# Performance work log

Measured on AMD Instinct MI355X. Metric: run time of the kernel, lower is better.

The kernel has to match this reference:

```python
import jax, jax.numpy as jnp
import numpy as np

NUM_HEADS = 16
WINDOW = 128


def apply_rope(x):
    # x: (B, H, S, Dh), standard RoPE with half-split rotation, base 10000
    S, Dh = x.shape[-2], x.shape[-1]
    half = Dh // 2
    inv_freq = 1.0 / (10000.0 ** (jnp.arange(half, dtype=jnp.float32) / half))
    ang = jnp.arange(S, dtype=jnp.float32)[:, None] * inv_freq[None, :]  # (S, half)
    cos, sin = jnp.cos(ang), jnp.sin(ang)
    x1, x2 = x[..., :half], x[..., half:]
    return jnp.concatenate([x1 * cos - x2 * sin, x1 * sin + x2 * cos], axis=-1).astype(x.dtype)


def setup_inputs() -> dict:
    key = jax.random.key(0)
    ks = jax.random.split(key, 5)
    D = 1024
    B, S = 2, 2048
    w = 0.02
    return {
        "x": jax.random.normal(ks[0], (B, S, D), dtype=jnp.float32),
        "Wq": jax.random.normal(ks[1], (D, D), dtype=jnp.float32) * w,
        "bq": jnp.zeros((D,), dtype=jnp.float32),
        "Wk": jax.random.normal(ks[2], (D, D), dtype=jnp.float32) * w,
        "bk": jnp.zeros((D,), dtype=jnp.float32),
        "Wv": jax.random.normal(ks[3], (D, D), dtype=jnp.float32) * w,
        "bv": jnp.zeros((D,), dtype=jnp.float32),
        "Wo": jax.random.normal(ks[4], (D, D), dtype=jnp.float32) * w,
        "bo": jnp.zeros((D,), dtype=jnp.float32),
    }


def reference(x, Wq, bq, Wk, bk, Wv, bv, Wo, bo):
    B, S, D = x.shape
    H = NUM_HEADS
    Dh = D // H

    def proj(W, b):
        y = jnp.einsum("bsd,ed->bse", x, W) + b  # nn.Linear: x @ W.T + b
        return y.reshape(B, S, H, Dh).transpose(0, 2, 1, 3)  # (B,H,S,Dh)

    q = apply_rope(proj(Wq, bq)) * (Dh ** -0.5)
    k = apply_rope(proj(Wk, bk))
    v = proj(Wv, bv)

    scores = jnp.einsum("bhqd,bhkd->bhqk", q, k)  # (B,H,S,S)
    idx = jnp.arange(S)
    rel = idx[None, :] - idx[:, None]  # k - q
    blocked = (rel > 0) | (rel < -WINDOW)  # True = masked out
    scores = jnp.where(blocked[None, None], -jnp.inf, scores)
    probs = jax.nn.softmax(scores, axis=-1)
    out = jnp.einsum("bhqk,bhkd->bhqd", probs, v)
    out = out.transpose(0, 2, 1, 3).reshape(B, S, D)
    return jnp.einsum("bsd,ed->bse", out, Wo) + bo
```

## Files before the change

### kernel.cpp

```cpp
#include <hip/hip_runtime.h>

typedef __attribute__((ext_vector_type(8)))  __bf16 bf16x8;
typedef __attribute__((ext_vector_type(4)))  float  f32x4;

__device__ __forceinline__ short f2bf(float f) {
    unsigned u = __builtin_bit_cast(unsigned, f);
    unsigned r = (u + 0x7fffu + ((u >> 16) & 1u)) >> 16;
    return (short)r;
}
__device__ __forceinline__ float lo16(unsigned u) { return __builtin_bit_cast(float, u << 16); }
__device__ __forceinline__ float hi16(unsigned u) { return __builtin_bit_cast(float, u & 0xffff0000u); }

__device__ __forceinline__ void gload16(const void* g, void* l) {
    __builtin_amdgcn_global_load_lds(
        (const __attribute__((address_space(1))) unsigned*)g,
        (__attribute__((address_space(3))) unsigned*)l, 16, 0, 0);
}

__device__ __forceinline__ void ropePair(const uint4& a, const uint4& b,
                                         const float2* cs8, float scale,
                                         uint4& oa, uint4& ob) {
    const unsigned au[4] = {a.x, a.y, a.z, a.w}, bu[4] = {b.x, b.y, b.z, b.w};
    unsigned ra[4], rb[4];
    #pragma unroll
    for (int wi = 0; wi < 4; ++wi) {
        const float x1l = lo16(au[wi]), x1h = hi16(au[wi]);
        const float x2l = lo16(bu[wi]), x2h = hi16(bu[wi]);
        const float2 cl = cs8[wi * 2], ch = cs8[wi * 2 + 1];
        const float o1l = (x1l * cl.x - x2l * cl.y) * scale;
        const float o2l = (x1l * cl.y + x2l * cl.x) * scale;
        const float o1h = (x1h * ch.x - x2h * ch.y) * scale;
        const float o2h = (x1h * ch.y + x2h * ch.x) * scale;
        ra[wi] = (unsigned)(unsigned short)f2bf(o1l) | ((unsigned)(unsigned short)f2bf(o1h) << 16);
        rb[wi] = (unsigned)(unsigned short)f2bf(o2l) | ((unsigned)(unsigned short)f2bf(o2h) << 16);
    }
    oa = make_uint4(ra[0], ra[1], ra[2], ra[3]);
    ob = make_uint4(rb[0], rb[1], rb[2], rb[3]);
}

#define S_LEN   2048
#define MAT_ELEMS 4194304
#define VT_ROW  2176
#define VT_MAT  2228224

__global__ __launch_bounds__(256) void prep(
    const float* __restrict__ x,  const float* __restrict__ Wq,
    const float* __restrict__ Wk, const float* __restrict__ Wv,
    const float* __restrict__ Wo, const float* __restrict__ bq,
    const float* __restrict__ bk, const float* __restrict__ bv,
    short* __restrict__ xb, short* __restrict__ wcat, short* __restrict__ wob,
    float* __restrict__ bcat, float2* __restrict__ tab, short* __restrict__ vt)
{
    const int tid = blockIdx.x * 256 + threadIdx.x;
    const float4* src;
    short* dst;
    if (tid < 1048576) {
        src = (const float4*)x + tid;  dst = xb + (size_t)tid * 4;
    } else if (tid < 1835008) {
        const int o = tid - 1048576;
        const int mat = o >> 18;
        const int wi  = o & 262143;
        const float* W = (mat == 0) ? Wq : (mat == 1) ? Wk : Wv;
        src = (const float4*)W + wi;  dst = wcat + (size_t)o * 4;
    } else {
        const int o = tid - 1835008;
        src = (const float4*)Wo + o;  dst = wob + (size_t)o * 4;
    }
    const float4 v = *src;
    short4 s4 = make_short4(f2bf(v.x), f2bf(v.y), f2bf(v.z), f2bf(v.w));
    *(short4*)dst = s4;

    if (tid < 65536) {
        const int s  = tid >> 5;
        const int jr = tid & 31;
        const float freq = exp2f(-(float)jr * (13.287712379549449f / 32.0f));
        const float ang  = (float)s * freq;
        tab[tid] = make_float2(cosf(ang), sinf(ang));
    }
    if (tid < 768) {
        const float* B = (tid < 256) ? bq : (tid < 512) ? bk : bv;
        ((float4*)bcat)[tid] = ((const float4*)B)[tid & 255];
    }
    if (tid < 16384) {
        const int row = tid >> 3, ch = tid & 7;
        *(uint4*)&vt[(size_t)row * VT_ROW + ch * 8] = make_uint4(0, 0, 0, 0);
    }
}

#define VMC4 do { asm volatile("s_waitcnt vmcnt(4)" ::: "memory"); __builtin_amdgcn_sched_barrier(0); } while (0)
#define VMC0 do { asm volatile("s_waitcnt vmcnt(0)" ::: "memory"); __builtin_amdgcn_sched_barrier(0); } while (0)
#define BAR  __builtin_amdgcn_s_barrier()
#define SB   __builtin_amdgcn_sched_barrier(0)

#define LDA_ALL(T) _Pragma("unroll") for (int ii = 0; ii < 4; ++ii) { \
    aF[ii][0] = ldf(T, fA0, ii * 2048);                                \
    aF[ii][1] = ldf(T, fA1, ii * 2048); }
#define LDB0(T) _Pragma("unroll") for (int jj = 0; jj < 3; ++jj) {    \
    b0[jj][0] = ldf(T, fB0, jj * 2048);                                \
    b0[jj][1] = ldf(T, fB1, jj * 2048); }
#define LDB1(T) _Pragma("unroll") for (int jj = 0; jj < 3; ++jj) {    \
    b1[jj][0] = ldf(T, fB0, (jj + 3) * 2048);                          \
    b1[jj][1] = ldf(T, fB1, (jj + 3) * 2048); }

#define MFMA_HALF(JB, BQ)                                                     \
  __builtin_amdgcn_s_setprio(1);                                              \
  _Pragma("unroll") for (int ii = 0; ii < 4; ++ii)                            \
    _Pragma("unroll") for (int jj = 0; jj < 3; ++jj) {                        \
      acc[ii][(JB)+jj] = __builtin_amdgcn_mfma_f32_16x16x32_bf16(             \
          aF[ii][0], BQ[jj][0], acc[ii][(JB)+jj], 0, 0, 0);                   \
      acc[ii][(JB)+jj] = __builtin_amdgcn_mfma_f32_16x16x32_bf16(             \
          aF[ii][1], BQ[jj][1], acc[ii][(JB)+jj], 0, 0, 0);                   \
    }                                                                         \
  __builtin_amdgcn_s_setprio(0);

#define STGA(KT_, TILE) _Pragma("unroll") for (int g = 0; g < 4; ++g)  \
    gload16(gA + g * 16384 + (KT_) * 128, (TILE) + (w * 32 + g * 8) * 64);
#define STGB(KT_, TILE) _Pragma("unroll") for (int g = 0; g < 3; ++g)  \
    gload16(gB + g * 16384 + (KT_) * 128, (TILE) + (w * 24 + g * 8) * 64);

#define KT2(CA, CB, SBSTG, SASTG, WSTMT)              \
  LDA_ALL(CA); LDB0(CB); SBSTG;                       \
  MFMA_HALF(0, b0); SB; LDB1(CB); SB;                 \
  BAR;                                                \
  SASTG;                                              \
  MFMA_HALF(3, b1); WSTMT; BAR;

__global__ __launch_bounds__(512) void gemm8(
    const short* __restrict__ A,
    const short* __restrict__ Bw,
    const float* __restrict__ bias,
    short* __restrict__ outb,
    short* __restrict__ vt)
{
    __shared__ short lds[57344];
    short* const Ab0 = lds;
    short* const Bb0 = lds + 16384;
    short* const Ab1 = lds + 28672;
    short* const Bb1 = lds + 45056;

    const int tid = threadIdx.x;
    const int w = tid >> 6, lane = tid & 63;
    const int wm = w >> 1, wn = w & 1;
    const int lr = lane & 15, lg = lane >> 4;

    const int wg  = blockIdx.x;
    const int swz = (wg & 7) * 32 + (wg >> 3);
    const int bx = swz & 15, by = swz >> 4;
    const int row0 = by * 256, col0 = bx * 192;

    const int scl  = ((lane & 7) * 16) ^ (((lane >> 3) & 7) << 4);
    const int goff = (lane >> 3) * 2048 + scl;
    const char* gA = (const char*)A  + (size_t)(row0 + w * 32) * 2048 + goff;
    const char* gB = (const char*)Bw + (size_t)(col0 + w * 24) * 2048 + goff;
    const int cswz0 = (lg * 16)      ^ ((lr & 7) << 4);
    const int cswz1 = (64 + lg * 16) ^ ((lr & 7) << 4);
    const int fA0 = (wm * 64 + lr) * 128 + cswz0;
    const int fA1 = (wm * 64 + lr) * 128 + cswz1;
    const int fB0 = (wn * 96 + lr) * 128 + cswz0;
    const int fB1 = (wn * 96 + lr) * 128 + cswz1;

    auto ldf = [&](const short* buf, int voff, int imm) -> bf16x8 {
        return *(const bf16x8*)((const char*)buf + voff + imm);
    };

    f32x4 acc[4][6] = {};
    bf16x8 aF[4][2], b0[3][2], b1[3][2];

    STGA(0, Ab0); STGB(0, Bb0); STGA(1, Ab1);
    VMC4;
    BAR;

    #pragma unroll 1
    for (int it = 0; it < 7; ++it) {
        const int t0 = it * 2;
        KT2(Ab0, Bb0, STGB(t0 + 1, Bb1), STGA(t0 + 2, Ab0), VMC4)
        const int t1 = t0 + 1;
        KT2(Ab1, Bb1, STGB(t1 + 1, Bb0), STGA(t1 + 2, Ab1), VMC4)
    }
    KT2(Ab0, Bb0, STGB(15, Bb1), {}, VMC0)
    KT2(Ab1, Bb1, {}, {}, {})

    #pragma unroll
    for (int j = 0; j < 6; ++j) {
        const int base_cm = col0 + wn * 96 + j * 16;
        const int matj = base_cm >> 10;
        const float bb = bias[base_cm + lr];
        if (matj == 2) {
            const size_t dgo = (size_t)(base_cm - 2048 + lr) * VT_ROW;
            #pragma unroll
            for (int i = 0; i < 4; ++i) {
                const int rg = row0 + wm * 64 + i * 16 + lg * 4;
                const int bq_ = rg >> 11, key = rg & 2047;
                short4 sv;
                sv.x = f2bf(acc[i][j][0] + bb); sv.y = f2bf(acc[i][j][1] + bb);
                sv.z = f2bf(acc[i][j][2] + bb); sv.w = f2bf(acc[i][j][3] + bb);
                *(short4*)&vt[(size_t)bq_ * VT_MAT + dgo + 128 + key] = sv;
            }
        } else {
            short* outm = outb + (size_t)matj * MAT_ELEMS;
            const int cmod = (base_cm & 1023) + lr;
            #pragma unroll
            for (int i = 0; i < 4; ++i) {
                const int rg = row0 + wm * 64 + i * 16 + lg * 4;
                #pragma unroll
                for (int r = 0; r < 4; ++r)
                    outm[(size_t)(rg + r) * 1024 + cmod] = f2bf(acc[i][j][r] + bb);
            }
        }
    }
}

__global__ __launch_bounds__(256) void gemm_out(
    const short* __restrict__ A, const short* __restrict__ Bw,
    const float* __restrict__ bias, float* __restrict__ outf)
{
    __shared__ short As[128 * 64];
    __shared__ short Bs[64 * 64];
    const int tid  = threadIdx.x;
    const int w    = tid >> 6, lane = tid & 63;
    const int row0 = blockIdx.y * 128, col0 = blockIdx.x * 64;
    const int lr   = lane & 15, lg = lane >> 4;
    const int srow = lane >> 3, scol = (lane & 7) * 8;

    f32x4 acc[2][4] = {};

    for (int kt = 0; kt < 16; ++kt) {
        const int k0 = kt * 64;
        __syncthreads();
        #pragma unroll
        for (int rr = 0; rr < 4; ++rr) {
            const int r = w * 32 + rr * 8;
            gload16(A + (size_t)(row0 + r + srow) * 1024 + k0 + scol, (short*)As + r * 64);
        }
        #pragma unroll
        for (int rr = 0; rr < 2; ++rr) {
            const int r = w * 16 + rr * 8;
            gload16(Bw + (size_t)(col0 + r + srow) * 1024 + k0 + scol, (short*)Bs + r * 64);
        }
        __syncthreads();
        #pragma unroll
        for (int kk = 0; kk < 2; ++kk) {
            const int kb = kk * 32 + lg * 8;
            bf16x8 af[2], bf[4];
            #pragma unroll
            for (int i = 0; i < 2; ++i)
                af[i] = *(const bf16x8*)&As[(w * 32 + i * 16 + lr) * 64 + kb];
            #pragma unroll
            for (int j = 0; j < 4; ++j)
                bf[j] = *(const bf16x8*)&Bs[(j * 16 + lr) * 64 + kb];
            #pragma unroll
            for (int i = 0; i < 2; ++i)
                #pragma unroll
                for (int j = 0; j < 4; ++j)
                    acc[i][j] = __builtin_amdgcn_mfma_f32_16x16x32_bf16(af[i], bf[j], acc[i][j], 0, 0, 0);
        }
    }

    #pragma unroll
    for (int i = 0; i < 2; ++i) {
        const int grb = row0 + w * 32 + i * 16 + lg * 4;
        #pragma unroll
        for (int j = 0; j < 4; ++j) {
            const int cm = col0 + j * 16 + lr;
            const float bb = bias[cm];
            #pragma unroll
            for (int r = 0; r < 4; ++r)
                outf[(size_t)(grb + r) * 1024 + cm] = acc[i][j][r] + bb;
        }
    }
}

#define KS_ST 72
#define P_ST  168
__global__ __launch_bounds__(512) void attn_mfma(const short* __restrict__ qkv,
                                                 const short* __restrict__ vt,
                                                 short* __restrict__ ctx,
                                                 const float2* __restrict__ tab)
{
    __shared__ char lds[76800];
    short* Ks  = (short*)lds;
    short* Pl  = (short*)lds;
    char*  VTs = lds + 43008;
    float* linv = (float*)(lds + 75776);

    const int tid = threadIdx.x;
    const int w = tid >> 6, lane = tid & 63;
    const int g = lane >> 4, l15 = lane & 15;
    const int phys = blockIdx.x;
    const int bid = (phys & 7) * 64 + (phys >> 3);
    const int b  = bid >> 8;
    const int h  = (bid >> 4) & 15;
    const int qb = bid & 15;
    const int qs = qb << 7;
    const size_t rowbase = (size_t)b * S_LEN;
    const int hc = h << 6;

    const short* vhead = vt + ((size_t)b * 1024 + h * 64) * VT_ROW + qs;
    #pragma unroll
    for (int rdx = 0; rdx < 4; ++rdx) {
        const int c = rdx * 512 + tid;
        const int row = c >> 5, ch = c & 31;
        const int srcb = (ch * 16) ^ ((row & 7) << 4);
        gload16((const char*)(vhead + (size_t)row * VT_ROW) + srcb, VTs + c * 16);
    }

    #pragma unroll
    for (int it = 0; it < 2; ++it) {
        const int c   = it * 512 + tid;
        const int key = c >> 2;
        const int jb  = (c & 3) << 3;
        const int gk  = qs - 128 + key;
        const int gkc = gk < 0 ? 0 : gk;
        const short* kb = qkv + (size_t)1 * MAT_ELEMS + (rowbase + gkc) * 1024 + hc;
        const uint4 k1 = *(const uint4*)(kb + jb);
        const uint4 k2 = *(const uint4*)(kb + jb + 32);
        uint4 o1, o2;
        ropePair(k1, k2, tab + (size_t)gkc * 32 + jb, 1.0f, o1, o2);
        if (gk < 0) { o1 = make_uint4(0, 0, 0, 0); o2 = make_uint4(0, 0, 0, 0); }
        *(uint4*)&Ks[key * KS_ST + jb]      = o1;
        *(uint4*)&Ks[key * KS_ST + jb + 32] = o2;
    }
    __syncthreads();

    const int q = qs + 16 * w + l15;
    const size_t qoff = (rowbase + q) * 1024 + hc;
    const uint4 q1 = *(const uint4*)&qkv[qoff + g * 8];
    const uint4 q2 = *(const uint4*)&qkv[qoff + 32 + g * 8];
    uint4 r1, r2;
    ropePair(q1, q2, tab + (size_t)q * 32 + g * 8, 0.125f, r1, r2);
    const bf16x8 qf0 = __builtin_bit_cast(bf16x8, r1);
    const bf16x8 qf1 = __builtin_bit_cast(bf16x8, r2);

    f32x4 st[9];
    #pragma unroll
    for (int t = 0; t < 9; ++t) {
        const int krow = 16 * w + 16 * t + l15;
        bf16x8 kf0 = *(const bf16x8*)&Ks[krow * KS_ST + g * 8];
        bf16x8 kf1 = *(const bf16x8*)&Ks[krow * KS_ST + 32 + g * 8];
        f32x4 a = {0.f, 0.f, 0.f, 0.f};
        a = __builtin_amdgcn_mfma_f32_16x16x32_bf16(qf0, kf0, a, 0, 0, 0);
        a = __builtin_amdgcn_mfma_f32_16x16x32_bf16(qf1, kf1, a, 0, 0, 0);
        st[t] = a;
    }
    __syncthreads();

    const int jmin = 128 - qs - 16 * w;
    float mrow[4], lsum[4];
    #pragma unroll
    for (int r = 0; r < 4; ++r) mrow[r] = -3.0e38f;
    #pragma unroll
    for (int t = 0; t < 9; ++t) {
        const int jj = 16 * t + l15;
        #pragma unroll
        for (int r = 0; r < 4; ++r) {
            const int qi = 4 * g + r;
            const bool ok = (jj >= qi) && (jj <= qi + 128) && (jj >= jmin);
            if (ok) mrow[r] = fmaxf(mrow[r], st[t][r]);
        }
    }
    #pragma unroll
    for (int r = 0; r < 4; ++r) {
        mrow[r] = fmaxf(mrow[r], __shfl_xor(mrow[r], 1));
        mrow[r] = fmaxf(mrow[r], __shfl_xor(mrow[r], 2));
        mrow[r] = fmaxf(mrow[r], __shfl_xor(mrow[r], 4));
        mrow[r] = fmaxf(mrow[r], __shfl_xor(mrow[r], 8));
        lsum[r] = 0.0f;
    }
    short* Pw = Pl + w * (16 * P_ST);
    #pragma unroll
    for (int t = 0; t < 9; ++t) {
        const int jj = 16 * t + l15;
        #pragma unroll
        for (int r = 0; r < 4; ++r) {
            const int qi = 4 * g + r;
            const bool ok = (jj >= qi) && (jj <= qi + 128) && (jj >= jmin);
            const float p = ok ? __expf(st[t][r] - mrow[r]) : 0.0f;
            lsum[r] += p;
            Pw[qi * P_ST + jj] = f2bf(p);
        }
    }
    {
        short4 z = make_short4(0, 0, 0, 0);
        *(short4*)&Pw[l15 * P_ST + 144 + 4 * g] = z;
    }
    #pragma unroll
    for (int r = 0; r < 4; ++r) {
        lsum[r] += __shfl_xor(lsum[r], 1);
        lsum[r] += __shfl_xor(lsum[r], 2);
        lsum[r] += __shfl_xor(lsum[r], 4);
        lsum[r] += __shfl_xor(lsum[r], 8);
        if (l15 == r) linv[w * 16 + 4 * g + r] = 1.0f / lsum[r];
    }

    f32x4 oc[4] = {};
    #pragma unroll
    for (int kc = 0; kc < 5; ++kc) {
        bf16x8 pf = *(const bf16x8*)&Pw[l15 * P_ST + kc * 32 + g * 8];
        int cole = 16 * w + kc * 32 + g * 8;
        if (cole > 248) cole = 248;
        const int colb = cole * 2;
        #pragma unroll
        for (int dt = 0; dt < 4; ++dt) {
            const int row = dt * 16 + l15;
            bf16x8 vf = *(const bf16x8*)(VTs + row * 512 + (colb ^ ((row & 7) << 4)));
            oc[dt] = __builtin_amdgcn_mfma_f32_16x16x32_bf16(vf, pf, oc[dt], 0, 0, 0);
        }
    }

    const float inv = linv[w * 16 + l15];
    #pragma unroll
    for (int dt = 0; dt < 4; ++dt) {
        short4 sv;
        sv.x = f2bf(oc[dt][0] * inv);
        sv.y = f2bf(oc[dt][1] * inv);
        sv.z = f2bf(oc[dt][2] * inv);
        sv.w = f2bf(oc[dt][3] * inv);
        *(short4*)&ctx[(rowbase + qs + 16 * w + l15) * 1024 + hc + dt * 16 + 4 * g] = sv;
    }
}

extern "C" void kernel_launch(void* const* d_in, const int* in_sizes, int n_in,
                              void* d_out, int out_size, void* d_ws, size_t ws_size,
                              hipStream_t stream) {
    const float* x  = (const float*)d_in[0];
    const float* Wq = (const float*)d_in[1];
    const float* bq = (const float*)d_in[2];
    const float* Wk = (const float*)d_in[3];
    const float* bk = (const float*)d_in[4];
    const float* Wv = (const float*)d_in[5];
    const float* bv = (const float*)d_in[6];
    const float* Wo = (const float*)d_in[7];
    const float* bo = (const float*)d_in[8];

    char* ws = (char*)d_ws;
    short*  xb   = (short*) (ws + 0);
    short*  ctx  = (short*) (ws + 0);
    short*  wcat = (short*) (ws + 8388608);
    short*  wob  = (short*) (ws + 14680064);
    short*  qkv  = (short*) (ws + 16777216);
    short*  vt   = (short*) (ws + 33554432);
    float2* tab  = (float2*)(ws + 42467328);
    float*  bcat = (float*) (ws + 42991616);

    prep<<<8192, 256, 0, stream>>>(x, Wq, Wk, Wv, Wo, bq, bk, bv,
                                   xb, wcat, wob, bcat, tab, vt);
    gemm8<<<256, 512, 0, stream>>>(xb, wcat, bcat, qkv, vt);
    attn_mfma<<<512, 512, 0, stream>>>(qkv, vt, ctx, tab);
    gemm_out<<<dim3(16, 32), 256, 0, stream>>>(ctx, wob, bo, (float*)d_out);
}
```

Baseline: 80.74 us.

## Split GEMM k-step into four barrier-separated LDS-load/MFMA phases

Restructures the QKV projection GEMM main loop so each k-tile is processed in four quarters. Each quarter loads half of the A or B fragments from LDS and then runs a 2x3 MFMA block, with workgroup barriers between phases in a ping-pong style schedule. The aim is to interleave LDS reads with MFMA work across waves and reduce register pressure from holding all A fragments at once. The cost is many more s_barrier calls per k-step, and the explicit sched_barrier hints are removed.

```diff
diff --git a/kernel.cpp b/kernel.cpp
--- a/kernel.cpp
+++ b/kernel.cpp
@@ -90,26 +90,28 @@
 #define VMC4 do { asm volatile("s_waitcnt vmcnt(4)" ::: "memory"); __builtin_amdgcn_sched_barrier(0); } while (0)
 #define VMC0 do { asm volatile("s_waitcnt vmcnt(0)" ::: "memory"); __builtin_amdgcn_sched_barrier(0); } while (0)
 #define BAR  __builtin_amdgcn_s_barrier()
-#define SB   __builtin_amdgcn_sched_barrier(0)
-
-#define LDA_ALL(T) _Pragma("unroll") for (int ii = 0; ii < 4; ++ii) { \
-    aF[ii][0] = ldf(T, fA0, ii * 2048);                                \
+
+#define LDAL(T) _Pragma("unroll") for (int ii = 0; ii < 2; ++ii) { \
+    aF[ii][0] = ldf(T, fA0, ii * 2048);                             \
     aF[ii][1] = ldf(T, fA1, ii * 2048); }
-#define LDB0(T) _Pragma("unroll") for (int jj = 0; jj < 3; ++jj) {    \
-    b0[jj][0] = ldf(T, fB0, jj * 2048);                                \
+#define LDAH(T) _Pragma("unroll") for (int ii = 2; ii < 4; ++ii) { \
+    aF[ii][0] = ldf(T, fA0, ii * 2048);                             \
+    aF[ii][1] = ldf(T, fA1, ii * 2048); }
+#define LDBL(T) _Pragma("unroll") for (int jj = 0; jj < 3; ++jj) { \
+    b0[jj][0] = ldf(T, fB0, jj * 2048);                             \
     b0[jj][1] = ldf(T, fB1, jj * 2048); }
-#define LDB1(T) _Pragma("unroll") for (int jj = 0; jj < 3; ++jj) {    \
-    b1[jj][0] = ldf(T, fB0, (jj + 3) * 2048);                          \
+#define LDBH(T) _Pragma("unroll") for (int jj = 0; jj < 3; ++jj) { \
+    b1[jj][0] = ldf(T, fB0, (jj + 3) * 2048);                       \
     b1[jj][1] = ldf(T, fB1, (jj + 3) * 2048); }
 
-#define MFMA_HALF(JB, BQ)                                                     \
+#define MFQ(IB, JB, BQ)                                                       \
   __builtin_amdgcn_s_setprio(1);                                              \
-  _Pragma("unroll") for (int ii = 0; ii < 4; ++ii)                            \
+  _Pragma("unroll") for (int ii = 0; ii < 2; ++ii)                            \
     _Pragma("unroll") for (int jj = 0; jj < 3; ++jj) {                        \
-      acc[ii][(JB)+jj] = __builtin_amdgcn_mfma_f32_16x16x32_bf16(             \
-          aF[ii][0], BQ[jj][0], acc[ii][(JB)+jj], 0, 0, 0);                   \
-      acc[ii][(JB)+jj] = __builtin_amdgcn_mfma_f32_16x16x32_bf16(             \
-          aF[ii][1], BQ[jj][1], acc[ii][(JB)+jj], 0, 0, 0);                   \
+      acc[(IB)+ii][(JB)+jj] = __builtin_amdgcn_mfma_f32_16x16x32_bf16(        \
+          aF[(IB)+ii][0], BQ[jj][0], acc[(IB)+ii][(JB)+jj], 0, 0, 0);         \
+      acc[(IB)+ii][(JB)+jj] = __builtin_amdgcn_mfma_f32_16x16x32_bf16(        \
+          aF[(IB)+ii][1], BQ[jj][1], acc[(IB)+ii][(JB)+jj], 0, 0, 0);         \
     }                                                                         \
   __builtin_amdgcn_s_setprio(0);
 
@@ -118,12 +120,11 @@
 #define STGB(KT_, TILE) _Pragma("unroll") for (int g = 0; g < 3; ++g)  \
     gload16(gB + g * 16384 + (KT_) * 128, (TILE) + (w * 24 + g * 8) * 64);
 
-#define KT2(CA, CB, SBSTG, SASTG, WSTMT)              \
-  LDA_ALL(CA); LDB0(CB); SBSTG;                       \
-  MFMA_HALF(0, b0); SB; LDB1(CB); SB;                 \
-  BAR;                                                \
-  SASTG;                                              \
-  MFMA_HALF(3, b1); WSTMT; BAR;
+#define KT8(CA, CB, SBSTG, SASTG, WSTMT)                  \
+  LDAL(CA); LDBL(CB); SBSTG; BAR; MFQ(0, 0, b0); BAR;     \
+  LDBH(CB);           BAR; MFQ(0, 3, b1); BAR;            \
+  LDAH(CA);           BAR; MFQ(2, 0, b0); BAR;            \
+  SASTG; WSTMT;       BAR; MFQ(2, 3, b1); BAR;
 
 __global__ __launch_bounds__(512) void gemm8(
     const short* __restrict__ A,
@@ -173,12 +174,12 @@
     #pragma unroll 1
     for (int it = 0; it < 7; ++it) {
         const int t0 = it * 2;
-        KT2(Ab0, Bb0, STGB(t0 + 1, Bb1), STGA(t0 + 2, Ab0), VMC4)
+        KT8(Ab0, Bb0, STGB(t0 + 1, Bb1), STGA(t0 + 2, Ab0), VMC4)
         const int t1 = t0 + 1;
-        KT2(Ab1, Bb1, STGB(t1 + 1, Bb0), STGA(t1 + 2, Ab1), VMC4)
-    }
-    KT2(Ab0, Bb0, STGB(15, Bb1), {}, VMC0)
-    KT2(Ab1, Bb1, {}, {}, {})
+        KT8(Ab1, Bb1, STGB(t1 + 1, Bb0), STGA(t1 + 2, Ab1), VMC4)
+    }
+    KT8(Ab0, Bb0, STGB(15, Bb1), {}, VMC0)
+    KT8(Ab1, Bb1, {}, {}, {})
 
     #pragma unroll
     for (int j = 0; j < 6; ++j) {
```

New measurement: 80.63 us. Within noise of the previous version (-0.1%).

## Replace pipelined 256x192 QKV GEMM with simple single-buffered 128x64 tiles

Applied to the files above, without the earlier changes.

The QKV projection GEMM drops its double-buffered 256x192 tile, 8-wave design with manual waitcnt and priority scheduling. In its place is a plain 128x64 tile per 4-wave block, loading each k-step into LDS between two __syncthreads. The grid goes from 256 to 1536 blocks, which gives more blocks per CU and better balance across the CUs, with an XCD-aware block mapping. The cost is lower data reuse per block and no overlap of global loads with MFMA work.

```diff
diff --git a/kernel.cpp b/kernel.cpp
--- a/kernel.cpp
+++ b/kernel.cpp
@@ -87,124 +87,89 @@
     }
 }
 
-#define VMC4 do { asm volatile("s_waitcnt vmcnt(4)" ::: "memory"); __builtin_amdgcn_sched_barrier(0); } while (0)
-#define VMC0 do { asm volatile("s_waitcnt vmcnt(0)" ::: "memory"); __builtin_amdgcn_sched_barrier(0); } while (0)
-#define BAR  __builtin_amdgcn_s_barrier()
-#define SB   __builtin_amdgcn_sched_barrier(0)
-
-#define LDA_ALL(T) _Pragma("unroll") for (int ii = 0; ii < 4; ++ii) { \
-    aF[ii][0] = ldf(T, fA0, ii * 2048);                                \
-    aF[ii][1] = ldf(T, fA1, ii * 2048); }
-#define LDB0(T) _Pragma("unroll") for (int jj = 0; jj < 3; ++jj) {    \
-    b0[jj][0] = ldf(T, fB0, jj * 2048);                                \
-    b0[jj][1] = ldf(T, fB1, jj * 2048); }
-#define LDB1(T) _Pragma("unroll") for (int jj = 0; jj < 3; ++jj) {    \
-    b1[jj][0] = ldf(T, fB0, (jj + 3) * 2048);                          \
-    b1[jj][1] = ldf(T, fB1, (jj + 3) * 2048); }
-
-#define MFMA_HALF(JB, BQ)                                                     \
-  __builtin_amdgcn_s_setprio(1);                                              \
-  _Pragma("unroll") for (int ii = 0; ii < 4; ++ii)                            \
-    _Pragma("unroll") for (int jj = 0; jj < 3; ++jj) {                        \
-      acc[ii][(JB)+jj] = __builtin_amdgcn_mfma_f32_16x16x32_bf16(             \
-          aF[ii][0], BQ[jj][0], acc[ii][(JB)+jj], 0, 0, 0);                   \
-      acc[ii][(JB)+jj] = __builtin_amdgcn_mfma_f32_16x16x32_bf16(             \
-          aF[ii][1], BQ[jj][1], acc[ii][(JB)+jj], 0, 0, 0);                   \
-    }                                                                         \
-  __builtin_amdgcn_s_setprio(0);
-
-#define STGA(KT_, TILE) _Pragma("unroll") for (int g = 0; g < 4; ++g)  \
-    gload16(gA + g * 16384 + (KT_) * 128, (TILE) + (w * 32 + g * 8) * 64);
-#define STGB(KT_, TILE) _Pragma("unroll") for (int g = 0; g < 3; ++g)  \
-    gload16(gB + g * 16384 + (KT_) * 128, (TILE) + (w * 24 + g * 8) * 64);
-
-#define KT2(CA, CB, SBSTG, SASTG, WSTMT)              \
-  LDA_ALL(CA); LDB0(CB); SBSTG;                       \
-  MFMA_HALF(0, b0); SB; LDB1(CB); SB;                 \
-  BAR;                                                \
-  SASTG;                                              \
-  MFMA_HALF(3, b1); WSTMT; BAR;
-
-__global__ __launch_bounds__(512) void gemm8(
+__global__ __launch_bounds__(256) void gemm8(
     const short* __restrict__ A,
     const short* __restrict__ Bw,
     const float* __restrict__ bias,
     short* __restrict__ outb,
     short* __restrict__ vt)
 {
-    __shared__ short lds[57344];
-    short* const Ab0 = lds;
-    short* const Bb0 = lds + 16384;
-    short* const Ab1 = lds + 28672;
-    short* const Bb1 = lds + 45056;
-
-    const int tid = threadIdx.x;
-    const int w = tid >> 6, lane = tid & 63;
-    const int wm = w >> 1, wn = w & 1;
-    const int lr = lane & 15, lg = lane >> 4;
+    __shared__ short As[128 * 64];
+    __shared__ short Bs[64 * 64];
+    const int tid  = threadIdx.x;
+    const int w    = tid >> 6, lane = tid & 63;
+    const int lr   = lane & 15, lg = lane >> 4;
 
     const int wg  = blockIdx.x;
-    const int swz = (wg & 7) * 32 + (wg >> 3);
-    const int bx = swz & 15, by = swz >> 4;
-    const int row0 = by * 256, col0 = bx * 192;
-
-    const int scl  = ((lane & 7) * 16) ^ (((lane >> 3) & 7) << 4);
-    const int goff = (lane >> 3) * 2048 + scl;
-    const char* gA = (const char*)A  + (size_t)(row0 + w * 32) * 2048 + goff;
-    const char* gB = (const char*)Bw + (size_t)(col0 + w * 24) * 2048 + goff;
+    const int xcd = wg & 7, i6 = wg >> 3;
+    const int by  = xcd * 4 + i6 / 48, bx = i6 % 48;
+    const int row0 = by * 128, col0 = bx * 64;
+
+    const int scl = ((lane & 7) * 16) ^ (((lane >> 3) & 7) << 4);
+    const char* gA = (const char*)A  + (size_t)(row0 + w * 32) * 2048 + (lane >> 3) * 2048 + scl;
+    const char* gB = (const char*)Bw + (size_t)(col0 + w * 16) * 2048 + (lane >> 3) * 2048 + scl;
     const int cswz0 = (lg * 16)      ^ ((lr & 7) << 4);
     const int cswz1 = (64 + lg * 16) ^ ((lr & 7) << 4);
-    const int fA0 = (wm * 64 + lr) * 128 + cswz0;
-    const int fA1 = (wm * 64 + lr) * 128 + cswz1;
-    const int fB0 = (wn * 96 + lr) * 128 + cswz0;
-    const int fB1 = (wn * 96 + lr) * 128 + cswz1;
-
-    auto ldf = [&](const short* buf, int voff, int imm) -> bf16x8 {
-        return *(const bf16x8*)((const char*)buf + voff + imm);
-    };
-
-    f32x4 acc[4][6] = {};
-    bf16x8 aF[4][2], b0[3][2], b1[3][2];
-
-    STGA(0, Ab0); STGB(0, Bb0); STGA(1, Ab1);
-    VMC4;
-    BAR;
-
-    #pragma unroll 1
-    for (int it = 0; it < 7; ++it) {
-        const int t0 = it * 2;
-        KT2(Ab0, Bb0, STGB(t0 + 1, Bb1), STGA(t0 + 2, Ab0), VMC4)
-        const int t1 = t0 + 1;
-        KT2(Ab1, Bb1, STGB(t1 + 1, Bb0), STGA(t1 + 2, Ab1), VMC4)
-    }
-    KT2(Ab0, Bb0, STGB(15, Bb1), {}, VMC0)
-    KT2(Ab1, Bb1, {}, {}, {})
-
-    #pragma unroll
-    for (int j = 0; j < 6; ++j) {
-        const int base_cm = col0 + wn * 96 + j * 16;
-        const int matj = base_cm >> 10;
-        const float bb = bias[base_cm + lr];
-        if (matj == 2) {
-            const size_t dgo = (size_t)(base_cm - 2048 + lr) * VT_ROW;
-            #pragma unroll
-            for (int i = 0; i < 4; ++i) {
-                const int rg = row0 + wm * 64 + i * 16 + lg * 4;
+
+    f32x4 acc[2][4] = {};
+
+    for (int kt = 0; kt < 16; ++kt) {
+        __syncthreads();
+        #pragma unroll
+        for (int rr = 0; rr < 4; ++rr)
+            gload16(gA + rr * 16384 + kt * 128, (short*)As + (w * 32 + rr * 8) * 64);
+        #pragma unroll
+        for (int rr = 0; rr < 2; ++rr)
+            gload16(gB + rr * 16384 + kt * 128, (short*)Bs + (w * 16 + rr * 8) * 64);
+        __syncthreads();
+        #pragma unroll
+        for (int kk = 0; kk < 2; ++kk) {
+            const int cs = kk ? cswz1 : cswz0;
+            bf16x8 af[2], bf[4];
+            #pragma unroll
+            for (int i = 0; i < 2; ++i)
+                af[i] = *(const bf16x8*)((const char*)As + (w * 32 + i * 16 + lr) * 128 + cs);
+            #pragma unroll
+            for (int j = 0; j < 4; ++j)
+                bf[j] = *(const bf16x8*)((const char*)Bs + (j * 16 + lr) * 128 + cs);
+            #pragma unroll
+            for (int i = 0; i < 2; ++i)
+                #pragma unroll
+                for (int j = 0; j < 4; ++j)
+                    acc[i][j] = __builtin_amdgcn_mfma_f32_16x16x32_bf16(af[i], bf[j], acc[i][j], 0, 0, 0);
+        }
+    }
+
+    const int mat = col0 >> 10;
+    const int cm0 = col0 & 1023;
+    if (mat == 2) {
+        #pragma unroll
+        for (int j = 0; j < 4; ++j) {
+            const int co = j * 16 + lr;
+            const float bb = bias[col0 + co];
+            const size_t dgo = (size_t)(cm0 + co) * VT_ROW;
+            #pragma unroll
+            for (int i = 0; i < 2; ++i) {
+                const int rg = row0 + w * 32 + i * 16 + lg * 4;
                 const int bq_ = rg >> 11, key = rg & 2047;
                 short4 sv;
                 sv.x = f2bf(acc[i][j][0] + bb); sv.y = f2bf(acc[i][j][1] + bb);
                 sv.z = f2bf(acc[i][j][2] + bb); sv.w = f2bf(acc[i][j][3] + bb);
                 *(short4*)&vt[(size_t)bq_ * VT_MAT + dgo + 128 + key] = sv;
             }
-        } else {
-            short* outm = outb + (size_t)matj * MAT_ELEMS;
-            const int cmod = (base_cm & 1023) + lr;
-            #pragma unroll
-            for (int i = 0; i < 4; ++i) {
-                const int rg = row0 + wm * 64 + i * 16 + lg * 4;
+        }
+    } else {
+        short* outm = outb + (size_t)mat * MAT_ELEMS;
+        #pragma unroll
+        for (int j = 0; j < 4; ++j) {
+            const int co = cm0 + j * 16 + lr;
+            const float bb = bias[col0 + j * 16 + lr];
+            #pragma unroll
+            for (int i = 0; i < 2; ++i) {
+                const int rg = row0 + w * 32 + i * 16 + lg * 4;
                 #pragma unroll
                 for (int r = 0; r < 4; ++r)
-                    outm[(size_t)(rg + r) * 1024 + cmod] = f2bf(acc[i][j][r] + bb);
+                    outm[(size_t)(rg + r) * 1024 + co] = f2bf(acc[i][j][r] + bb);
             }
         }
     }
@@ -444,7 +409,7 @@
 
     prep<<<8192, 256, 0, stream>>>(x, Wq, Wk, Wv, Wo, bq, bk, bv,
                                    xb, wcat, wob, bcat, tab, vt);
-    gemm8<<<256, 512, 0, stream>>>(xb, wcat, bcat, qkv, vt);
+    gemm8<<<1536, 256, 0, stream>>>(xb, wcat, bcat, qkv, vt);
     attn_mfma<<<512, 512, 0, stream>>>(qkv, vt, ctx, tab);
     gemm_out<<<dim3(16, 32), 256, 0, stream>>>(ctx, wob, bo, (float*)d_out);
 }
```

Result: slower. 89.30 us (+10.6%).
